# Kernel optimization log

Measured on AMD Instinct MI355X. Metric: run time of the kernel, lower is better.

## Reference

```python
import jax, jax.numpy as jnp
import numpy as np
from jax import lax

LEVEL = 128  # level_num

def _bn(x, g, b, m, v):
    # inference-mode BatchNorm, channel axis = 1
    sh = (1, -1) + (1,) * (x.ndim - 2)
    return (x - m.reshape(sh)) * (g.reshape(sh) * lax.rsqrt(v.reshape(sh) + 1e-5)) + b.reshape(sh)

def _leaky(a):
    return jnp.where(a > 0, a, 0.01 * a)

def _l2n(a):
    return a / jnp.maximum(jnp.linalg.norm(a, axis=1, keepdims=True), 1e-12)

def _resize_bilinear_ac(x, oh, ow):
    # bilinear, align_corners=True, NCHW
    n, c, h, w = x.shape
    ys = jnp.linspace(0.0, h - 1.0, oh)
    xs = jnp.linspace(0.0, w - 1.0, ow)
    y0 = jnp.floor(ys).astype(jnp.int32)
    x0 = jnp.floor(xs).astype(jnp.int32)
    y1 = jnp.minimum(y0 + 1, h - 1)
    x1 = jnp.minimum(x0 + 1, w - 1)
    wy = (ys - y0)[:, None]
    wx = (xs - x0)[None, :]
    Y0, Y1, X0, X1 = y0[:, None], y1[:, None], x0[None, :], x1[None, :]
    return (x[:, :, Y0, X0] * (1 - wy) * (1 - wx) + x[:, :, Y0, X1] * (1 - wy) * wx
            + x[:, :, Y1, X0] * wy * (1 - wx) + x[:, :, Y1, X1] * wy * wx)

def _forward(x, conv1_w, bn1_g, bn1_b, bn1_m, bn1_v, conv2_w, f1_w, f2_w, f2_g, f2_b, f2_m, f2_v,
             out1_w, out1_g, out1_b, out1_m, out1_v, k_w, q_w, v_w, out_w, out_g, out_b, out_m, out_v):
    # conv1: 3x3 conv + BN + LeakyReLU
    y = lax.conv_general_dilated(x, conv1_w, (1, 1), 'SAME', dimension_numbers=('NCHW', 'OIHW', 'NCHW'))
    y = _leaky(_bn(y, bn1_g, bn1_b, bn1_m, bn1_v))
    # conv2: 1x1 conv, 256->128
    x2 = jnp.einsum('nchw,oc->nohw', y, conv2_w)
    N, C, H, W = x2.shape  # C = 128
    x_ave = x2.mean(axis=(2, 3), keepdims=True)  # [N,C,1,1]
    cos = (_l2n(x_ave) * _l2n(x2)).sum(1)        # [N,H,W]
    sh, sw = H // 3, W // 3
    L = sh * sw
    # H,W divisible by 3 -> adaptive_avg_pool2d is identity
    cs = cos.reshape(N, 3, sh, 3, sw).transpose(0, 1, 3, 2, 4).reshape(N, 9, L).transpose(0, 2, 1)  # [N,L,9]
    # LBP bit packing vs center (index 4); weight 0 at index 4 (strict > gives 0 there)
    bits = (cs > cs[:, :, 4:5]).astype(x.dtype)
    wts = jnp.array([1, 2, 4, 8, 0, 16, 32, 64, 128], dtype=x.dtype)
    code = (bits * wts).sum(-1)  # [N,L]
    mn = code.min(-1, keepdims=True)
    mx = code.max(-1, keepdims=True)
    code = (code - mn) / (mx - mn)
    cmin = code.min(-1, keepdims=True)
    cmax = code.max(-1, keepdims=True)
    qlv = (2 * jnp.arange(LEVEL, dtype=x.dtype) + 1) / (2 * LEVEL) * (cmax - cmin) + cmin  # [N,LEVEL]
    inter = (qlv[:, 1] - qlv[:, 0])[:, None, None]  # [N,1,1]
    quant = 1 - jnp.abs(qlv[:, None, :] - code[:, :, None])  # [N,L,LEVEL]
    quant = jnp.where(quant > 1 - inter, quant, 0.0)
    sta = quant.sum(1)                                       # [N,LEVEL]
    sta = sta / sta.sum(-1, keepdims=True)
    sta2 = jnp.stack([qlv, sta], axis=1)                     # [N,2,LEVEL]
    h1 = _leaky(jnp.einsum('ncl,oc->nol', sta2, f1_w))       # f1: 2->64
    h2 = jax.nn.relu(_bn(jnp.einsum('ncl,oc->nol', h1, f2_w), f2_g, f2_b, f2_m, f2_v))  # f2: 64->128
    xa = jnp.broadcast_to(x_ave[:, :, 0, 0][:, :, None], (N, C, LEVEL))
    s = jnp.concatenate([h2, xa], axis=1)                    # [N,256,LEVEL]
    s = jax.nn.relu(_bn(jnp.einsum('ncl,oc->nol', s, out1_w), out1_g, out1_b, out1_m, out1_v))
    k = jnp.einsum('ncl,oc->nol', s, k_w)
    q = jnp.einsum('ncl,oc->nol', s, q_w)
    v = jnp.einsum('ncl,oc->nol', s, v_w)
    w = jax.nn.softmax(jnp.einsum('ncl,ncm->nlm', k, q), axis=-1)  # bmm(k^T, q)
    f = jnp.einsum('nlm,ncm->ncl', w, v)                            # bmm(w, v^T) then transpose
    f = jax.nn.relu(_bn(jnp.einsum('ncl,oc->nol', f, out_w), out_g, out_b, out_m, out_v))
    out = jnp.einsum('ncl,npl->ncp', f, quant).reshape(N, 256, sh, sh)  # bmm(f, quant^T)
    return _resize_bilinear_ac(out, H, W)

def setup_inputs() -> dict:
    key = jax.random.key(0)
    ks = jax.random.split(key, 16)
    f32 = jnp.float32
    def nrm(k, shape, s=0.05):
        return s * jax.random.normal(k, shape, f32)
    def bnp(k, c):
        k1, k2, k3, k4 = jax.random.split(k, 4)
        return (1.0 + 0.1 * jax.random.normal(k1, (c,), f32),
                0.1 * jax.random.normal(k2, (c,), f32),
                0.1 * jax.random.normal(k3, (c,), f32),
                jax.random.uniform(k4, (c,), f32, 0.5, 1.5))
    d = {}
    d['x'] = jax.random.normal(ks[0], (32, 512, 48, 48), f32)
    d['conv1_w'] = nrm(ks[1], (256, 512, 3, 3))
    d['bn1_g'], d['bn1_b'], d['bn1_m'], d['bn1_v'] = bnp(ks[2], 256)
    d['conv2_w'] = nrm(ks[3], (128, 256))
    d['f1_w'] = nrm(ks[4], (64, 2), 0.3)
    d['f2_w'] = nrm(ks[5], (128, 64), 0.1)
    d['f2_g'], d['f2_b'], d['f2_m'], d['f2_v'] = bnp(ks[6], 128)
    d['out1_w'] = nrm(ks[7], (256, 256))
    d['out1_g'], d['out1_b'], d['out1_m'], d['out1_v'] = bnp(ks[8], 256)
    d['k_w'] = nrm(ks[9], (256, 256))
    d['q_w'] = nrm(ks[10], (256, 256))
    d['v_w'] = nrm(ks[11], (256, 256))
    d['out_w'] = nrm(ks[12], (256, 256))
    d['out_g'], d['out_b'], d['out_m'], d['out_v'] = bnp(ks[13], 256)
    return d

def reference(x, conv1_w, bn1_g, bn1_b, bn1_m, bn1_v, conv2_w, f1_w, f2_w, f2_g, f2_b, f2_m, f2_v,
              out1_w, out1_g, out1_b, out1_m, out1_v, k_w, q_w, v_w, out_w, out_g, out_b, out_m, out_v):
    return _forward(x, conv1_w, bn1_g, bn1_b, bn1_m, bn1_v, conv2_w, f1_w, f2_w, f2_g, f2_b, f2_m, f2_v,
                    out1_w, out1_g, out1_b, out1_m, out1_v, k_w, q_w, v_w, out_w, out_g, out_b, out_m, out_v)
```

## Files before the change

### kernel.cpp

```cpp
#include <hip/hip_runtime.h>
#include <math.h>

#define N_IMG 32
#define P2304 2304
#define CIN 512
#define CMID 256
#define C2 128
#define LEV 128

typedef _Float16 half8 __attribute__((ext_vector_type(8)));
typedef float f32x16 __attribute__((ext_vector_type(16)));
typedef unsigned short u16;
typedef unsigned int u32;

__device__ __forceinline__ float wredSum(float v){
#pragma unroll
  for (int o = 32; o > 0; o >>= 1) v += __shfl_down(v, o, 64);
  return v;
}
__device__ __forceinline__ float wredMax(float v){
#pragma unroll
  for (int o = 32; o > 0; o >>= 1) v = fmaxf(v, __shfl_down(v, o, 64));
  return v;
}
__device__ __forceinline__ float wredMin(float v){
#pragma unroll
  for (int o = 32; o > 0; o >>= 1) v = fminf(v, __shfl_down(v, o, 64));
  return v;
}

__device__ __forceinline__ void gll16(const void* g, void* l){
  __builtin_amdgcn_global_load_lds(
      (const __attribute__((address_space(1))) void*)g,
      (__attribute__((address_space(3))) void*)l, 16, 0, 0);
}

__global__ void prep_w1_kernel(const float* __restrict__ w1,
                               uint4* __restrict__ Wh, uint4* __restrict__ Wl){
  int fid = blockIdx.x * 256 + threadIdx.x;
  int lam = fid & 63;
  int c32 = (fid >> 6) & 3;
  int cot = (fid >> 8) & 1;
  int kt  = fid >> 9;
  int co = cot * 128 + c32 * 32 + (lam & 31);
  half8 vh, vl;
#pragma unroll
  for (int j = 0; j < 8; ++j){
    int k = kt * 16 + ((lam >> 5) << 3) + j;
    int r = k >> 9;
    int ci = k & 511;
    float v = w1[co * (CIN * 9) + ci * 9 + r];
    _Float16 h = (_Float16)v;
    vh[j] = h;
    vl[j] = (_Float16)((v - (float)h) * 2048.0f);
  }
  Wh[fid] = *(uint4*)&vh;
  Wl[fid] = *(uint4*)&vl;
}

__global__ void prep_w2_kernel(const float* __restrict__ w2,
                               uint4* __restrict__ Wh, uint4* __restrict__ Wl){
  int fid = blockIdx.x * 256 + threadIdx.x;
  int lam = fid & 63;
  int c32 = (fid >> 6) & 3;
  int kt  = fid >> 8;
  int co = c32 * 32 + (lam & 31);
  half8 vh, vl;
#pragma unroll
  for (int j = 0; j < 8; ++j){
    int k = kt * 16 + ((lam >> 5) << 3) + j;
    float v = w2[co * CMID + k];
    _Float16 h = (_Float16)v;
    vh[j] = h;
    vl[j] = (_Float16)((v - (float)h) * 2048.0f);
  }
  Wh[fid] = *(uint4*)&vh;
  Wl[fid] = *(uint4*)&vl;
}

__global__ void prep_bn_kernel(const float* __restrict__ g1, const float* __restrict__ b1,
                               const float* __restrict__ m1, const float* __restrict__ v1,
                               float* __restrict__ s1, float* __restrict__ t1){
  int c = threadIdx.x;
  float s = g1[c] * (1.0f / sqrtf(v1[c] + 1e-5f));
  s1[c] = s;
  t1[c] = b1[c] - m1[c] * s;
}

__global__ void prep_x_kernel(const float* __restrict__ x,
                              u16* __restrict__ xh, u16* __restrict__ xl,
                              int n0){
  __shared__ float tile[128 * 49];
  const int t = threadIdx.x;
  const int b = blockIdx.x;
  const int n_loc = b / 50;
  const int hp = b - n_loc * 50;
  const int n = n0 + n_loc;
  const int h = hp - 1;
  const bool vrow = (h >= 0) && (h < 48);
  const size_t orow = ((size_t)n_loc * 50 + hp) * 50 * 512;
  for (int cc = 0; cc < 4; ++cc){
    if (vrow){
      const float* src = x + (((size_t)n * 512 + cc * 128) * 48 + h) * 48;
#pragma unroll
      for (int i = 0; i < 24; ++i){
        int idx = t + 256 * i;
        int w = idx % 48;
        int c = idx / 48;
        tile[c * 49 + w] = src[(size_t)c * 2304 + w];
      }
    }
    __syncthreads();
    for (int i = 0; i < 13; ++i){
      int idx = t + 256 * i;
      if (idx < 3200){
        int cpair = idx & 63;
        int wp = idx >> 6;
        int w = wp - 1;
        float v0 = 0.f, v1 = 0.f;
        if (vrow && (unsigned)w < 48u){
          v0 = tile[(cpair * 2) * 49 + w];
          v1 = tile[(cpair * 2 + 1) * 49 + w];
        }
        _Float16 h0 = (_Float16)v0, h1 = (_Float16)v1;
        _Float16 l0 = (_Float16)((v0 - (float)h0) * 2048.0f);
        _Float16 l1 = (_Float16)((v1 - (float)h1) * 2048.0f);
        union { _Float16 hh[2]; u32 uu; } ph, pl;
        ph.hh[0] = h0; ph.hh[1] = h1;
        pl.hh[0] = l0; pl.hh[1] = l1;
        ((u32*)(xh + orow + (size_t)wp * 512 + cc * 128))[cpair] = ph.uu;
        ((u32*)(xl + orow + (size_t)wp * 512 + cc * 128))[cpair] = pl.uu;
      }
    }
    __syncthreads();
  }
}

template<int NC>
__global__ __launch_bounds__(256, 2) void conv1_lds_kernel(
    const u16* __restrict__ xh, const u16* __restrict__ xl,
    const uint4* __restrict__ Wh, const uint4* __restrict__ Wl,
    const float* __restrict__ s1, const float* __restrict__ t1,
    float* __restrict__ out, int n0)
{
  __shared__ _Float16 Abuf[2][2][2][2048];
  __shared__ _Float16 Bbuf[2][2][2][2048];
  const int t = threadIdx.x;
  const int lam = t & 63;
  const int g = t >> 6;

  const int xcd = blockIdx.x & 7;
  const int rest = blockIdx.x >> 3;
  const int NPX = NC / 8;
  const int n_loc = xcd * NPX + rest / 36;
  const int inner = rest % 36;
  const int pt_blk = inner % 18;
  const int cot = inner / 18;
  const int n = n0 + n_loc;

  const int pbase = pt_blk * 128;
  const int khi = lam >> 5;
  const int pp = (g << 5) + (lam & 31);
  const int p = pbase + pp;
  const int ph = p / 48, pw = p - ph * 48;
  const u16* xh_n = xh + (size_t)n_loc * 1280000;
  const u16* xl_n = xl + (size_t)n_loc * 1280000;

  const int S = 144;

  f32x16 acc_hh[2][2], acc_x[2][2];
#pragma unroll
  for (int a = 0; a < 2; ++a)
#pragma unroll
    for (int b = 0; b < 2; ++b){
#pragma unroll
      for (int e = 0; e < 16; ++e){ acc_hh[a][b][e] = 0.f; acc_x[a][b][e] = 0.f; }
    }

#define ISSUE_L(SV, BUF)                                                      \
  {                                                                           \
    int s_ = (SV);                                                            \
    int k0_ = 2 * s_;                                                         \
    _Pragma("unroll")                                                         \
    for (int kf = 0; kf < 2; ++kf){                                           \
      int fg_ = ((k0_ + kf) * 2 + cot) * 4 + g;                               \
      gll16(Wh + fg_ * 64 + lam, &Abuf[BUF][kf][0][t * 8]);                   \
      gll16(Wl + fg_ * 64 + lam, &Abuf[BUF][kf][1][t * 8]);                   \
    }                                                                         \
    int r_ = k0_ >> 5;                                          \
    int cb_ = (k0_ & 31) << 4;                       \
    int hh_ = ph + r_ / 3;                                    \
    int ww_ = pw + r_ % 3;                                    \
    const u16* sh_ = xh_n + ((hh_ * 50 + ww_) << 9) + cb_ + (khi << 3);       \
    const u16* sl_ = xl_n + ((hh_ * 50 + ww_) << 9) + cb_ + (khi << 3);       \
    _Pragma("unroll")                                                         \
    for (int kf = 0; kf < 2; ++kf){                                           \
      gll16(sh_ + kf * 16, &Bbuf[BUF][kf][0][t * 8]);                         \
      gll16(sl_ + kf * 16, &Bbuf[BUF][kf][1][t * 8]);                         \
    }                                                                         \
  }

#define COMPUTE_L(CUR, KF)                                                    \
  {                                                                           \
    const int ct0 = (g & 1) * 2, pt0 = (g >> 1) * 2;                          \
    half8 fAh[2], fAl[2], fBh[2], fBl[2];                                     \
    _Pragma("unroll")                                                         \
    for (int a = 0; a < 2; ++a){                                              \
      fAh[a] = *(half8*)&Abuf[CUR][KF][0][(ct0 + a) * 512 + lam * 8];         \
      fAl[a] = *(half8*)&Abuf[CUR][KF][1][(ct0 + a) * 512 + lam * 8];         \
      fBh[a] = *(half8*)&Bbuf[CUR][KF][0][(pt0 + a) * 512 + lam * 8];         \
      fBl[a] = *(half8*)&Bbuf[CUR][KF][1][(pt0 + a) * 512 + lam * 8];         \
    }                                                                         \
    _Pragma("unroll")                                                         \
    for (int a = 0; a < 2; ++a)                                               \
      _Pragma("unroll")                                                       \
      for (int b = 0; b < 2; ++b){                                            \
        acc_hh[a][b] = __builtin_amdgcn_mfma_f32_32x32x16_f16(                \
            fAh[a], fBh[b], acc_hh[a][b], 0, 0, 0);                           \
        acc_x[a][b] = __builtin_amdgcn_mfma_f32_32x32x16_f16(                 \
            fAh[a], fBl[b], acc_x[a][b], 0, 0, 0);                            \
        acc_x[a][b] = __builtin_amdgcn_mfma_f32_32x32x16_f16(                 \
            fAl[a], fBh[b], acc_x[a][b], 0, 0, 0);                            \
      }                                                                       \
  }

  ISSUE_L(0, 0);
  __syncthreads();

  for (int s = 0; s < S; ++s){
    const int cur = s & 1;
    if (s + 1 < S) ISSUE_L(s + 1, cur ^ 1);
    COMPUTE_L(cur, 0);
    COMPUTE_L(cur, 1);
    __syncthreads();
  }
#undef ISSUE_L
#undef COMPUTE_L

  const int cobase = cot * 128;
#pragma unroll
  for (int a = 0; a < 2; ++a){
    const int ctile = (g & 1) * 2 + a;
#pragma unroll
    for (int b = 0; b < 2; ++b){
      const int ptile = (g >> 1) * 2 + b;
      const int pg = pbase + ptile * 32 + (lam & 31);
#pragma unroll
      for (int rg = 0; rg < 16; ++rg){
        const int row = (rg & 3) + 8 * (rg >> 2) + 4 * (lam >> 5);
        const int co = cobase + ctile * 32 + row;
        float val = acc_hh[a][b][rg] + acc_x[a][b][rg] * (1.0f / 2048.0f);
        val = val * s1[co] + t1[co];
        val = val > 0.f ? val : 0.01f * val;
        out[((size_t)n * 256 + co) * P2304 + pg] = val;
      }
    }
  }
}

template<int R, int CPT, int COTN, bool BN>
__global__ __launch_bounds__(256, 2) void conv_mfma_kernel(
    const float* __restrict__ in, const uint4* __restrict__ Wh, const uint4* __restrict__ Wl,
    const float* __restrict__ s1, const float* __restrict__ t1, float* __restrict__ out)
{
  __shared__ _Float16 Abuf[2][2][2][2048];
  __shared__ _Float16 Bbuf[2][2][2][2048];
  const int t = threadIdx.x;
  const int lam = t & 63;
  const int g = t >> 6;

  int n, pt_blk, cot;
  if (COTN == 2){
    int xcd = blockIdx.x & 7;
    int rest = blockIdx.x >> 3;
    n = xcd * 4 + rest / 36;
    int inner = rest % 36;
    pt_blk = inner % 18;
    cot = inner / 18;
  } else {
    pt_blk = blockIdx.x % 18;
    cot = 0;
    n = blockIdx.x / 18;
  }
  const int pbase = pt_blk * 128;
  const int cobase = cot * 128;

  const int khi = lam >> 5;
  const int pp = (g << 5) + (lam & 31);
  const int p = pbase + pp;
  const int ph = p / 48, pw = p - ph * 48;
  const float* in_n = in + (size_t)n * CPT * P2304;

  const int S = (R * CPT) / 32;
  const int KTPT = CPT / 16;

  f32x16 acc_hh[2][2], acc_x[2][2];
#pragma unroll
  for (int a = 0; a < 2; ++a)
#pragma unroll
    for (int b = 0; b < 2; ++b){
#pragma unroll
      for (int e = 0; e < 16; ++e){ acc_hh[a][b][e] = 0.f; acc_x[a][b][e] = 0.f; }
    }

  uint4 rAh[2], rAl[2];
  float rB[16];
  bool vmask;

#define ISSUE(SV)                                                             \
  {                                                                           \
    int s_ = (SV);                                                            \
    _Pragma("unroll")                                                         \
    for (int kf = 0; kf < 2; ++kf){                                           \
      int fi = (((2 * s_ + kf) * COTN + cot) * 4 + g) * 64 + lam;             \
      rAh[kf] = Wh[fi];                                                       \
      rAl[kf] = Wl[fi];                                                       \
    }                                                                         \
    int r_ = (R == 1) ? 0 : ((2 * s_) / KTPT);                                \
    int cbase_ = ((2 * s_) % KTPT) * 16;                                      \
    int dh_ = (R == 1) ? 0 : (r_ / 3 - 1);                                    \
    int dw_ = (R == 1) ? 0 : (r_ - (r_ / 3) * 3 - 1);                         \
    int hh_ = ph + dh_, ww_ = pw + dw_;                                       \
    vmask = ((unsigned)hh_ < 48u) & ((unsigned)ww_ < 48u);                    \
    int hc_ = min(max(hh_, 0), 47), wc_ = min(max(ww_, 0), 47);               \
    const float* src_ = in_n + hc_ * 48 + wc_                                 \
                        + (size_t)(cbase_ + khi * 8) * P2304;                 \
    _Pragma("unroll")                                                         \
    for (int kf = 0; kf < 2; ++kf)                                            \
      _Pragma("unroll")                                                       \
      for (int j = 0; j < 8; ++j)                                             \
        rB[kf * 8 + j] = src_[(kf * 16 + j) * P2304];                         \
  }

#define STASH(NXT)                                                            \
  {                                                                           \
    _Pragma("unroll")                                                         \
    for (int kf = 0; kf < 2; ++kf){                                           \
      *(uint4*)&Abuf[NXT][kf][0][t * 8] = rAh[kf];                            \
      *(uint4*)&Abuf[NXT][kf][1][t * 8] = rAl[kf];                            \
      half8 vh, vl;                                                           \
      _Pragma("unroll")                                                       \
      for (int j = 0; j < 8; ++j){                                            \
        float v = vmask ? rB[kf * 8 + j] : 0.0f;                              \
        _Float16 h = (_Float16)v;                                             \
        vh[j] = h;                                                            \
        vl[j] = (_Float16)((v - (float)h) * 2048.0f);                         \
      }                                                                       \
      *(half8*)&Bbuf[NXT][kf][0][t * 8] = vh;                                 \
      *(half8*)&Bbuf[NXT][kf][1][t * 8] = vl;                                 \
    }                                                                         \
  }

#define COMPUTE(CUR, KF)                                                      \
  {                                                                           \
    const int ct0 = (g & 1) * 2, pt0 = (g >> 1) * 2;                          \
    half8 fAh[2], fAl[2], fBh[2], fBl[2];                                     \
    _Pragma("unroll")                                                         \
    for (int a = 0; a < 2; ++a){                                              \
      fAh[a] = *(half8*)&Abuf[CUR][KF][0][(ct0 + a) * 512 + lam * 8];         \
      fAl[a] = *(half8*)&Abuf[CUR][KF][1][(ct0 + a) * 512 + lam * 8];         \
      fBh[a] = *(half8*)&Bbuf[CUR][KF][0][(pt0 + a) * 512 + lam * 8];         \
      fBl[a] = *(half8*)&Bbuf[CUR][KF][1][(pt0 + a) * 512 + lam * 8];         \
    }                                                                         \
    _Pragma("unroll")                                                         \
    for (int a = 0; a < 2; ++a)                                               \
      _Pragma("unroll")                                                       \
      for (int b = 0; b < 2; ++b){                                            \
        acc_hh[a][b] = __builtin_amdgcn_mfma_f32_32x32x16_f16(                \
            fAh[a], fBh[b], acc_hh[a][b], 0, 0, 0);                           \
        acc_x[a][b] = __builtin_amdgcn_mfma_f32_32x32x16_f16(                 \
            fAh[a], fBl[b], acc_x[a][b], 0, 0, 0);                            \
        acc_x[a][b] = __builtin_amdgcn_mfma_f32_32x32x16_f16(                 \
            fAl[a], fBh[b], acc_x[a][b], 0, 0, 0);                            \
      }                                                                       \
  }

  ISSUE(0);
  STASH(0);
  __syncthreads();

  for (int s = 0; s < S; ++s){
    const int cur = s & 1, nxt = cur ^ 1;
    const bool more = (s + 1 < S);
    if (more) ISSUE(s + 1);
    COMPUTE(cur, 0);
    if (more) STASH(nxt);
    COMPUTE(cur, 1);
    __syncthreads();
  }
#undef ISSUE
#undef STASH
#undef COMPUTE

  const int M = COTN * 128;
#pragma unroll
  for (int a = 0; a < 2; ++a){
    const int ctile = (g & 1) * 2 + a;
#pragma unroll
    for (int b = 0; b < 2; ++b){
      const int ptile = (g >> 1) * 2 + b;
      const int pg = pbase + ptile * 32 + (lam & 31);
#pragma unroll
      for (int rg = 0; rg < 16; ++rg){
        const int row = (rg & 3) + 8 * (rg >> 2) + 4 * (lam >> 5);
        const int co = cobase + ctile * 32 + row;
        float val = acc_hh[a][b][rg] + acc_x[a][b][rg] * (1.0f / 2048.0f);
        if (BN){
          val = val * s1[co] + t1[co];
          val = val > 0.f ? val : 0.01f * val;
        }
        out[((size_t)n * M + co) * P2304 + pg] = val;
      }
    }
  }
}

__global__ void xave_kernel(const float* __restrict__ x2, float* __restrict__ xave){
  __shared__ float red[4];
  int nc = blockIdx.x, t = threadIdx.x;
  const float* row = x2 + nc * P2304;
  float s = 0.f;
#pragma unroll
  for (int i = 0; i < 9; i++) s += row[t + 256 * i];
  float w = wredSum(s);
  if ((t & 63) == 0) red[t >> 6] = w;
  __syncthreads();
  if (t == 0) xave[nc] = (red[0] + red[1] + red[2] + red[3]) * (1.0f / 2304.0f);
}

__global__ void xan_kernel(const float* __restrict__ xave, float* __restrict__ xan){
  __shared__ float red[2];
  int n = blockIdx.x, t = threadIdx.x;
  float v = xave[n * 128 + t];
  float w = wredSum(v * v);
  if ((t & 63) == 0) red[t >> 6] = w;
  __syncthreads();
  float norm = fmaxf(sqrtf(red[0] + red[1]), 1e-12f);
  xan[n * 128 + t] = v / norm;
}

__global__ void cos_kernel(const float* __restrict__ x2, const float* __restrict__ xan,
                           float* __restrict__ cosb){
  int idx = blockIdx.x * 256 + threadIdx.x;
  if (idx >= N_IMG * P2304) return;
  int n = idx / P2304;
  int p = idx - n * P2304;
  const float* xp = x2 + n * C2 * P2304 + p;
  const float* an = xan + n * 128;
  float dot = 0.f, ss = 0.f;
  for (int c = 0; c < 128; c++){
    float v = xp[c * P2304];
    dot += an[c] * v;
    ss  += v * v;
  }
  cosb[idx] = dot / fmaxf(sqrtf(ss), 1e-12f);
}

__global__ void lbp_kernel(const float* __restrict__ cosb, float* __restrict__ code,
                           float* __restrict__ qlv){
  __shared__ float red[4];
  int n = blockIdx.x;
  int l = threadIdx.x;
  int ir = l >> 4, ic = l & 15;
  const float* cn = cosb + n * P2304;
  float cs4 = cn[(16 + ir) * 48 + (16 + ic)];
  const float wts[9] = {1.f, 2.f, 4.f, 8.f, 0.f, 16.f, 32.f, 64.f, 128.f};
  float codev = 0.f;
#pragma unroll
  for (int j = 0; j < 9; j++){
    int jr = j / 3, jc = j - 3 * (j / 3);
    float vv = cn[(jr * 16 + ir) * 48 + (jc * 16 + ic)];
    if (vv > cs4) codev += wts[j];
  }
  float w;
  w = wredMin(codev);
  if ((l & 63) == 0) red[l >> 6] = w;
  __syncthreads();
  float mn = fminf(fminf(red[0], red[1]), fminf(red[2], red[3]));
  __syncthreads();
  w = wredMax(codev);
  if ((l & 63) == 0) red[l >> 6] = w;
  __syncthreads();
  float mx = fmaxf(fmaxf(red[0], red[1]), fmaxf(red[2], red[3]));
  __syncthreads();
  float cd = (codev - mn) / (mx - mn);
  w = wredMin(cd);
  if ((l & 63) == 0) red[l >> 6] = w;
  __syncthreads();
  float cmin = fminf(fminf(red[0], red[1]), fminf(red[2], red[3]));
  __syncthreads();
  w = wredMax(cd);
  if ((l & 63) == 0) red[l >> 6] = w;
  __syncthreads();
  float cmax = fmaxf(fmaxf(red[0], red[1]), fmaxf(red[2], red[3]));
  code[n * 256 + l] = cd;
  if (l < 128){
    float tmp = (float)(2 * l + 1) * (1.0f / 256.0f);
    qlv[n * 128 + l] = tmp * (cmax - cmin) + cmin;
  }
}

__global__ void quant_kernel(const float* __restrict__ code, const float* __restrict__ qlv,
                             float* __restrict__ quantT){
  __shared__ float cs[256];
  __shared__ float qs[128];
  int n = blockIdx.x, t = threadIdx.x;
  cs[t] = code[n * 256 + t];
  if (t < 128) qs[t] = qlv[n * 128 + t];
  __syncthreads();
  float thr = 1.0f - (qs[1] - qs[0]);
  float* dst = quantT + n * LEV * 256;
#pragma unroll 4
  for (int i = 0; i < 128; i++){
    int v = t + 256 * i;
    int lv = v >> 8;
    int p = v & 255;
    float qq = 1.0f - fabsf(qs[lv] - cs[p]);
    dst[v] = (qq > thr) ? qq : 0.f;
  }
}

__global__ void sta_kernel(const float* __restrict__ quantT, float* __restrict__ sta){
  __shared__ float red[2];
  int n = blockIdx.x, i = threadIdx.x;
  const float* qr = quantT + (n * LEV + i) * 256;
  float s = 0.f;
  for (int p = 0; p < 256; p++) s += qr[p];
  float w = wredSum(s);
  if ((i & 63) == 0) red[i >> 6] = w;
  __syncthreads();
  float tot = red[0] + red[1];
  sta[n * 128 + i] = s / tot;
}

__global__ void h1_kernel(const float* __restrict__ f1w, const float* __restrict__ qlv,
                          const float* __restrict__ sta, float* __restrict__ h1){
  int idx = blockIdx.x * 256 + threadIdx.x;
  if (idx >= N_IMG * 64 * 128) return;
  int l = idx & 127;
  int n = idx >> 13;
  int o = (idx >> 7) & 63;
  float a = f1w[o * 2] * qlv[n * 128 + l] + f1w[o * 2 + 1] * sta[n * 128 + l];
  h1[idx] = a > 0.f ? a : 0.01f * a;
}

__global__ void gemm_w_kernel(const float* __restrict__ Wm, const float* __restrict__ B,
                              float* __restrict__ Cout, int Cdim, int O, int total, int mode,
                              const float* __restrict__ g, const float* __restrict__ bb,
                              const float* __restrict__ mm, const float* __restrict__ vv){
  int idx = blockIdx.x * 256 + threadIdx.x;
  if (idx >= total) return;
  int per_n = (O >> 2) << 7;
  int n = idx / per_n;
  int rem = idx - n * per_n;
  int o0 = (rem >> 7) << 2;
  int l = rem & 127;
  const float* Bn = B + (n * Cdim) * 128 + l;
  const float* w0 = Wm + (o0 + 0) * Cdim;
  const float* w1 = Wm + (o0 + 1) * Cdim;
  const float* w2 = Wm + (o0 + 2) * Cdim;
  const float* w3 = Wm + (o0 + 3) * Cdim;
  float a0 = 0, a1 = 0, a2 = 0, a3 = 0;
  for (int c = 0; c < Cdim; c++){
    float bv = Bn[c * 128];
    a0 += w0[c] * bv; a1 += w1[c] * bv; a2 += w2[c] * bv; a3 += w3[c] * bv;
  }
  float av[4] = {a0, a1, a2, a3};
#pragma unroll
  for (int j = 0; j < 4; j++){
    int o = o0 + j;
    float val = av[j];
    if (mode == 1){
      float s = g[o] * (1.0f / sqrtf(vv[o] + 1e-5f));
      val = (val - mm[o]) * s + bb[o];
      val = fmaxf(val, 0.f);
    }
    Cout[(n * O + o) * 128 + l] = val;
  }
}

__global__ void concat_kernel(const float* __restrict__ h2, const float* __restrict__ xave,
                              float* __restrict__ s){
  int idx = blockIdx.x * 256 + threadIdx.x;
  if (idx >= N_IMG * 256 * 128) return;
  int l = idx & 127;
  int c = (idx >> 7) & 255;
  int n = idx >> 15;
  s[idx] = (c < 128) ? h2[(n * 128 + c) * 128 + l] : xave[n * 128 + (c - 128)];
}

__global__ void attn_sc_kernel(const float* __restrict__ k, const float* __restrict__ q,
                               float* __restrict__ sc){
  int idx = blockIdx.x * 256 + threadIdx.x;
  if (idx >= N_IMG * 32 * 128) return;
  int m = idx & 127;
  int l0 = ((idx >> 7) & 31) << 2;
  int n = idx >> 12;
  const float* kn = k + n * 256 * 128;
  const float* qn = q + n * 256 * 128 + m;
  float a0 = 0, a1 = 0, a2 = 0, a3 = 0;
  for (int c = 0; c < 256; c++){
    float qv = qn[c * 128];
    const float* kr = kn + c * 128 + l0;
    a0 += kr[0] * qv; a1 += kr[1] * qv; a2 += kr[2] * qv; a3 += kr[3] * qv;
  }
  float* dst = sc + (n * 128 + l0) * 128 + m;
  dst[0] = a0; dst[128] = a1; dst[256] = a2; dst[384] = a3;
}

__global__ void softmax_kernel(float* __restrict__ sc){
  __shared__ float red[2];
  int row = blockIdx.x;
  int t = threadIdx.x;
  float v = sc[row * 128 + t];
  float w = wredMax(v);
  if ((t & 63) == 0) red[t >> 6] = w;
  __syncthreads();
  float mx = fmaxf(red[0], red[1]);
  float e = expf(v - mx);
  float s = wredSum(e);
  __syncthreads();
  if ((t & 63) == 0) red[t >> 6] = s;
  __syncthreads();
  sc[row * 128 + t] = e / (red[0] + red[1]);
}

__global__ void transpose_sc_kernel(const float* __restrict__ sc, float* __restrict__ scT){
  int idx = blockIdx.x * 256 + threadIdx.x;
  if (idx >= N_IMG * 128 * 128) return;
  int l = idx & 127;
  int m = (idx >> 7) & 127;
  int n = idx >> 14;
  scT[idx] = sc[(n * 128 + l) * 128 + m];
}

__global__ void attn_f_kernel(const float* __restrict__ vb, const float* __restrict__ scT,
                              float* __restrict__ f){
  int idx = blockIdx.x * 256 + threadIdx.x;
  if (idx >= N_IMG * 64 * 128) return;
  int l = idx & 127;
  int c0 = ((idx >> 7) & 63) << 2;
  int n = idx >> 13;
  const float* vn = vb + (n * 256 + c0) * 128;
  const float* sn = scT + n * 128 * 128 + l;
  float a0 = 0, a1 = 0, a2 = 0, a3 = 0;
  for (int m = 0; m < 128; m++){
    float sv = sn[m * 128];
    a0 += vn[m] * sv; a1 += vn[128 + m] * sv; a2 += vn[256 + m] * sv; a3 += vn[384 + m] * sv;
  }
  float* dst = f + (n * 256 + c0) * 128 + l;
  dst[0] = a0; dst[128] = a1; dst[256] = a2; dst[384] = a3;
}

__global__ void final_kernel(const float* __restrict__ g, const float* __restrict__ quantT,
                             float* __restrict__ outs){
  int idx = blockIdx.x * 256 + threadIdx.x;
  if (idx >= N_IMG * 64 * 256) return;
  int p = idx & 255;
  int c0 = ((idx >> 8) & 63) << 2;
  int n = idx >> 14;
  const float* gn = g + (n * 256 + c0) * 128;
  const float* qn = quantT + (n * LEV) * 256 + p;
  float a0 = 0, a1 = 0, a2 = 0, a3 = 0;
  for (int lv = 0; lv < 128; lv++){
    float qv = qn[lv * 256];
    a0 += gn[lv] * qv; a1 += gn[128 + lv] * qv; a2 += gn[256 + lv] * qv; a3 += gn[384 + lv] * qv;
  }
  float* dst = outs + (n * 256 + c0) * 256 + p;
  dst[0] = a0; dst[256] = a1; dst[512] = a2; dst[768] = a3;
}

__global__ void resize_kernel(const float* __restrict__ outs, float* __restrict__ dout){
  int idx = blockIdx.x * 256 + threadIdx.x;
  if (idx >= N_IMG * 256 * P2304) return;
  int ow = idx % 48;
  int tmp = idx / 48;
  int oh = tmp % 48;
  int nc = tmp / 48;
  const float* src = outs + nc * 256;
  float fy = oh * (15.0f / 47.0f);
  float fx = ow * (15.0f / 47.0f);
  int y0 = (int)fy;
  int x0 = (int)fx;
  int y1 = min(y0 + 1, 15);
  int x1 = min(x0 + 1, 15);
  float wy = fy - (float)y0;
  float wx = fx - (float)x0;
  float v00 = src[y0 * 16 + x0], v01 = src[y0 * 16 + x1];
  float v10 = src[y1 * 16 + x0], v11 = src[y1 * 16 + x1];
  dout[idx] = v00 * (1.f - wy) * (1.f - wx) + v01 * (1.f - wy) * wx
            + v10 * wy * (1.f - wx) + v11 * wy * wx;
}

extern "C" void kernel_launch(void* const* d_in, const int* in_sizes, int n_in,
                              void* d_out, int out_size, void* d_ws, size_t ws_size,
                              hipStream_t stream)
{
  const float* x       = (const float*)d_in[0];
  const float* conv1_w = (const float*)d_in[1];
  const float* bn1_g   = (const float*)d_in[2];
  const float* bn1_b   = (const float*)d_in[3];
  const float* bn1_m   = (const float*)d_in[4];
  const float* bn1_v   = (const float*)d_in[5];
  const float* conv2_w = (const float*)d_in[6];
  const float* f1_w    = (const float*)d_in[7];
  const float* f2_w    = (const float*)d_in[8];
  const float* f2_g    = (const float*)d_in[9];
  const float* f2_b    = (const float*)d_in[10];
  const float* f2_m    = (const float*)d_in[11];
  const float* f2_v    = (const float*)d_in[12];
  const float* out1_w  = (const float*)d_in[13];
  const float* out1_g  = (const float*)d_in[14];
  const float* out1_b  = (const float*)d_in[15];
  const float* out1_m  = (const float*)d_in[16];
  const float* out1_v  = (const float*)d_in[17];
  const float* k_w     = (const float*)d_in[18];
  const float* q_w     = (const float*)d_in[19];
  const float* v_w     = (const float*)d_in[20];
  const float* out_w   = (const float*)d_in[21];
  const float* out_g   = (const float*)d_in[22];
  const float* out_b   = (const float*)d_in[23];
  const float* out_m   = (const float*)d_in[24];
  const float* out_v   = (const float*)d_in[25];

  float* ws = (float*)d_ws;
  float* dout = (float*)d_out;

  float* w_y   = ws;
  float* w_x2  = ws + 18874368;
  float* w_W1h = ws + 28311552;
  float* w_W1l = ws + 28901376;
  float* w_W2h = ws + 29491200;
  float* w_W2l = ws + 29507584;
  float* w_s1  = ws + 29523968;
  float* w_t1  = ws + 29524224;
  float* w_xave = w_y + 0;
  float* w_xan  = w_y + 4096;
  float* w_cos  = w_y + 8192;
  float* w_code = w_y + 81920;
  float* w_qlv  = w_y + 90112;
  float* w_sta  = w_y + 94208;
  float* w_quant= w_y + 98304;
  float* w_h1   = w_y + 1146880;
  float* w_h2   = w_y + 1409024;
  float* w_s    = w_y + 1933312;
  float* w_k    = w_y + 2981888;
  float* w_q    = w_y + 4030464;
  float* w_v    = w_y + 5079040;
  float* w_sc   = w_y + 6127616;
  float* w_scT  = w_y + 6651904;
  float* w_f    = w_y + 7176192;
  float* w_g    = w_y + 8224768;
  float* w_outs = w_y + 9273344;
  float* w_s2   = w_y + 11370496;

  prep_w1_kernel<<<576, 256, 0, stream>>>(conv1_w, (uint4*)w_W1h, (uint4*)w_W1l);
  prep_w2_kernel<<<16, 256, 0, stream>>>(conv2_w, (uint4*)w_W2h, (uint4*)w_W2l);
  prep_bn_kernel<<<1, 256, 0, stream>>>(bn1_g, bn1_b, bn1_m, bn1_v, w_s1, w_t1);

  const size_t BASE_F = 29524480;
  const size_t XPI_F  = 640000;
  const size_t ws_f = ws_size / 4;
  int NCc = 0;
  if (ws_f >= BASE_F + 2 * 32 * XPI_F)      NCc = 32;
  else if (ws_f >= BASE_F + 2 * 16 * XPI_F) NCc = 16;

  if (NCc > 0){
    u16* w_xh = (u16*)(ws + BASE_F);
    u16* w_xl = w_xh + (size_t)NCc * 1280000;
    const int nchunk = N_IMG / NCc;
    for (int c = 0; c < nchunk; ++c){
      int n0 = c * NCc;
      prep_x_kernel<<<NCc * 50, 256, 0, stream>>>(x, w_xh, w_xl, n0);
      if (NCc == 32)
        conv1_lds_kernel<32><<<1152, 256, 0, stream>>>(
            w_xh, w_xl, (const uint4*)w_W1h, (const uint4*)w_W1l, w_s1, w_t1, w_y, n0);
      else
        conv1_lds_kernel<16><<<576, 256, 0, stream>>>(
            w_xh, w_xl, (const uint4*)w_W1h, (const uint4*)w_W1l, w_s1, w_t1, w_y, n0);
    }
  } else {
    conv_mfma_kernel<9, 512, 2, true><<<1152, 256, 0, stream>>>(
        x, (const uint4*)w_W1h, (const uint4*)w_W1l, w_s1, w_t1, w_y);
  }

  conv_mfma_kernel<1, 256, 1, false><<<576, 256, 0, stream>>>(
      w_y, (const uint4*)w_W2h, (const uint4*)w_W2l, w_s1, w_t1, w_x2);

  xave_kernel<<<4096, 256, 0, stream>>>(w_x2, w_xave);
  xan_kernel<<<32, 128, 0, stream>>>(w_xave, w_xan);
  cos_kernel<<<288, 256, 0, stream>>>(w_x2, w_xan, w_cos);
  lbp_kernel<<<32, 256, 0, stream>>>(w_cos, w_code, w_qlv);
  quant_kernel<<<32, 256, 0, stream>>>(w_code, w_qlv, w_quant);
  sta_kernel<<<32, 128, 0, stream>>>(w_quant, w_sta);
  h1_kernel<<<1024, 256, 0, stream>>>(f1_w, w_qlv, w_sta, w_h1);
  gemm_w_kernel<<<512, 256, 0, stream>>>(f2_w, w_h1, w_h2, 64, 128, N_IMG * 32 * 128, 1,
                                         f2_g, f2_b, f2_m, f2_v);
  concat_kernel<<<4096, 256, 0, stream>>>(w_h2, w_xave, w_s);
  gemm_w_kernel<<<1024, 256, 0, stream>>>(out1_w, w_s, w_s2, 256, 256, N_IMG * 64 * 128, 1,
                                          out1_g, out1_b, out1_m, out1_v);
  gemm_w_kernel<<<1024, 256, 0, stream>>>(k_w, w_s2, w_k, 256, 256, N_IMG * 64 * 128, 0,
                                          nullptr, nullptr, nullptr, nullptr);
  gemm_w_kernel<<<1024, 256, 0, stream>>>(q_w, w_s2, w_q, 256, 256, N_IMG * 64 * 128, 0,
                                          nullptr, nullptr, nullptr, nullptr);
  gemm_w_kernel<<<1024, 256, 0, stream>>>(v_w, w_s2, w_v, 256, 256, N_IMG * 64 * 128, 0,
                                          nullptr, nullptr, nullptr, nullptr);
  attn_sc_kernel<<<512, 256, 0, stream>>>(w_k, w_q, w_sc);
  softmax_kernel<<<4096, 128, 0, stream>>>(w_sc);
  transpose_sc_kernel<<<2048, 256, 0, stream>>>(w_sc, w_scT);
  attn_f_kernel<<<1024, 256, 0, stream>>>(w_v, w_scT, w_f);
  gemm_w_kernel<<<1024, 256, 0, stream>>>(out_w, w_f, w_g, 256, 256, N_IMG * 64 * 128, 1,
                                          out_g, out_b, out_m, out_v);
  final_kernel<<<2048, 256, 0, stream>>>(w_g, w_quant, w_outs);
  resize_kernel<<<73728, 256, 0, stream>>>(w_outs, dout);
}
```

Before: 1.736 ms.

## Deepen conv1 pipeline to 4 stages and emit split-fp16 NHWC for new conv2 kernel

The conv1 LDS kernel moves from a double-buffered loop with full __syncthreads to a four-slot ring. It prefetches two steps ahead, waits on explicit vmcnt counters with raw barriers, and raises wave priority around the MFMA block. The conv1 epilogue now writes its output as hi/lo fp16 pairs in pixel-major layout instead of fp32 NCHW. A new conv2 kernel then streams those pairs straight into LDS with direct global-to-LDS loads, removing the per-element fp32-to-fp16 split and staging conversion. This trades more LDS per block and hand-tuned wait counts, which are fragile, for better latency hiding and less conversion work between the two convolutions.

```diff
diff --git a/kernel.cpp b/kernel.cpp
--- a/kernel.cpp
+++ b/kernel.cpp
@@ -136,71 +136,7 @@
   }
 }
 
-template<int NC>
-__global__ __launch_bounds__(256, 2) void conv1_lds_kernel(
-    const u16* __restrict__ xh, const u16* __restrict__ xl,
-    const uint4* __restrict__ Wh, const uint4* __restrict__ Wl,
-    const float* __restrict__ s1, const float* __restrict__ t1,
-    float* __restrict__ out, int n0)
-{
-  __shared__ _Float16 Abuf[2][2][2][2048];
-  __shared__ _Float16 Bbuf[2][2][2][2048];
-  const int t = threadIdx.x;
-  const int lam = t & 63;
-  const int g = t >> 6;
-
-  const int xcd = blockIdx.x & 7;
-  const int rest = blockIdx.x >> 3;
-  const int NPX = NC / 8;
-  const int n_loc = xcd * NPX + rest / 36;
-  const int inner = rest % 36;
-  const int pt_blk = inner % 18;
-  const int cot = inner / 18;
-  const int n = n0 + n_loc;
-
-  const int pbase = pt_blk * 128;
-  const int khi = lam >> 5;
-  const int pp = (g << 5) + (lam & 31);
-  const int p = pbase + pp;
-  const int ph = p / 48, pw = p - ph * 48;
-  const u16* xh_n = xh + (size_t)n_loc * 1280000;
-  const u16* xl_n = xl + (size_t)n_loc * 1280000;
-
-  const int S = 144;
-
-  f32x16 acc_hh[2][2], acc_x[2][2];
-#pragma unroll
-  for (int a = 0; a < 2; ++a)
-#pragma unroll
-    for (int b = 0; b < 2; ++b){
-#pragma unroll
-      for (int e = 0; e < 16; ++e){ acc_hh[a][b][e] = 0.f; acc_x[a][b][e] = 0.f; }
-    }
-
-#define ISSUE_L(SV, BUF)                                                      \
-  {                                                                           \
-    int s_ = (SV);                                                            \
-    int k0_ = 2 * s_;                                                         \
-    _Pragma("unroll")                                                         \
-    for (int kf = 0; kf < 2; ++kf){                                           \
-      int fg_ = ((k0_ + kf) * 2 + cot) * 4 + g;                               \
-      gll16(Wh + fg_ * 64 + lam, &Abuf[BUF][kf][0][t * 8]);                   \
-      gll16(Wl + fg_ * 64 + lam, &Abuf[BUF][kf][1][t * 8]);                   \
-    }                                                                         \
-    int r_ = k0_ >> 5;                                          \
-    int cb_ = (k0_ & 31) << 4;                       \
-    int hh_ = ph + r_ / 3;                                    \
-    int ww_ = pw + r_ % 3;                                    \
-    const u16* sh_ = xh_n + ((hh_ * 50 + ww_) << 9) + cb_ + (khi << 3);       \
-    const u16* sl_ = xl_n + ((hh_ * 50 + ww_) << 9) + cb_ + (khi << 3);       \
-    _Pragma("unroll")                                                         \
-    for (int kf = 0; kf < 2; ++kf){                                           \
-      gll16(sh_ + kf * 16, &Bbuf[BUF][kf][0][t * 8]);                         \
-      gll16(sl_ + kf * 16, &Bbuf[BUF][kf][1][t * 8]);                         \
-    }                                                                         \
-  }
-
-#define COMPUTE_L(CUR, KF)                                                    \
+#define COMPUTE_M(CUR, KF)                                                    \
   {                                                                           \
     const int ct0 = (g & 1) * 2, pt0 = (g >> 1) * 2;                          \
     half8 fAh[2], fAl[2], fBh[2], fBl[2];                                     \
@@ -224,18 +160,100 @@
       }                                                                       \
   }
 
-  ISSUE_L(0, 0);
-  __syncthreads();
-
-  for (int s = 0; s < S; ++s){
-    const int cur = s & 1;
-    if (s + 1 < S) ISSUE_L(s + 1, cur ^ 1);
-    COMPUTE_L(cur, 0);
-    COMPUTE_L(cur, 1);
-    __syncthreads();
-  }
-#undef ISSUE_L
-#undef COMPUTE_L
+#define WAITV16 asm volatile("s_waitcnt vmcnt(16)" ::: "memory")
+#define WAITV8  asm volatile("s_waitcnt vmcnt(8)"  ::: "memory")
+#define WAITV0  asm volatile("s_waitcnt vmcnt(0)"  ::: "memory")
+#define BARSB { __builtin_amdgcn_s_barrier(); __builtin_amdgcn_sched_barrier(0); }
+
+template<int NC>
+__global__ __launch_bounds__(256, 2) void conv1_lds_kernel(
+    const u16* __restrict__ xh, const u16* __restrict__ xl,
+    const uint4* __restrict__ Wh, const uint4* __restrict__ Wl,
+    const float* __restrict__ s1, const float* __restrict__ t1,
+    u16* __restrict__ yh, u16* __restrict__ yl, int n0)
+{
+  __shared__ _Float16 Abuf[4][2][2][2048];
+  __shared__ _Float16 Bbuf[4][2][2][2048];
+  const int t = threadIdx.x;
+  const int lam = t & 63;
+  const int g = t >> 6;
+
+  const int xcd = blockIdx.x & 7;
+  const int rest = blockIdx.x >> 3;
+  const int NPX = NC / 8;
+  const int n_loc = xcd * NPX + rest / 36;
+  const int inner = rest % 36;
+  const int pt_blk = inner % 18;
+  const int cot = inner / 18;
+  const int n = n0 + n_loc;
+
+  const int pbase = pt_blk * 128;
+  const int khi = lam >> 5;
+  const int pp = (g << 5) + (lam & 31);
+  const int p = pbase + pp;
+  const int ph = p / 48, pw = p - ph * 48;
+  const u16* xh_n = xh + (size_t)n_loc * 1280000;
+  const u16* xl_n = xl + (size_t)n_loc * 1280000;
+
+  const int S = 144;
+
+  f32x16 acc_hh[2][2], acc_x[2][2];
+#pragma unroll
+  for (int a = 0; a < 2; ++a)
+#pragma unroll
+    for (int b = 0; b < 2; ++b){
+#pragma unroll
+      for (int e = 0; e < 16; ++e){ acc_hh[a][b][e] = 0.f; acc_x[a][b][e] = 0.f; }
+    }
+
+#define ISSUE1(SV, BUF)                                                       \
+  {                                                                           \
+    int s_ = (SV);                                                            \
+    int k0_ = 2 * s_;                                                         \
+    _Pragma("unroll")                                                         \
+    for (int kf = 0; kf < 2; ++kf){                                           \
+      int fg_ = ((k0_ + kf) * 2 + cot) * 4 + g;                               \
+      gll16(Wh + fg_ * 64 + lam, &Abuf[BUF][kf][0][t * 8]);                   \
+      gll16(Wl + fg_ * 64 + lam, &Abuf[BUF][kf][1][t * 8]);                   \
+    }                                                                         \
+    int r_ = k0_ >> 5;                                          \
+    int cb_ = (k0_ & 31) << 4;                       \
+    int hh_ = ph + r_ / 3;                                    \
+    int ww_ = pw + r_ % 3;                                    \
+    const u16* sh_ = xh_n + ((hh_ * 50 + ww_) << 9) + cb_ + (khi << 3);       \
+    const u16* sl_ = xl_n + ((hh_ * 50 + ww_) << 9) + cb_ + (khi << 3);       \
+    _Pragma("unroll")                                                         \
+    for (int kf = 0; kf < 2; ++kf){                                           \
+      gll16(sh_ + kf * 16, &Bbuf[BUF][kf][0][t * 8]);                         \
+      gll16(sl_ + kf * 16, &Bbuf[BUF][kf][1][t * 8]);                         \
+    }                                                                         \
+  }
+
+  ISSUE1(0, 0);
+  ISSUE1(1, 1);
+
+  for (int s = 0; s < S - 2; ++s){
+    ISSUE1(s + 2, (s + 2) & 3);
+    WAITV16;
+    BARSB;
+    __builtin_amdgcn_s_setprio(1);
+    COMPUTE_M(s & 3, 0);
+    COMPUTE_M(s & 3, 1);
+    __builtin_amdgcn_s_setprio(0);
+  }
+  WAITV8;
+  BARSB;
+  __builtin_amdgcn_s_setprio(1);
+  COMPUTE_M((S - 2) & 3, 0);
+  COMPUTE_M((S - 2) & 3, 1);
+  __builtin_amdgcn_s_setprio(0);
+  WAITV0;
+  BARSB;
+  __builtin_amdgcn_s_setprio(1);
+  COMPUTE_M((S - 1) & 3, 0);
+  COMPUTE_M((S - 1) & 3, 1);
+  __builtin_amdgcn_s_setprio(0);
+#undef ISSUE1
 
   const int cobase = cot * 128;
 #pragma unroll
@@ -245,14 +263,117 @@
     for (int b = 0; b < 2; ++b){
       const int ptile = (g >> 1) * 2 + b;
       const int pg = pbase + ptile * 32 + (lam & 31);
+      u16* dh = yh + (((size_t)n * P2304 + pg) << 8);
+      u16* dl = yl + (((size_t)n * P2304 + pg) << 8);
+#pragma unroll
+      for (int q = 0; q < 4; ++q){
+        const int co0 = cobase + ctile * 32 + 8 * q + 4 * khi;
+        union { _Float16 h[4]; uint2 u; } Uh, Ul;
+#pragma unroll
+        for (int i = 0; i < 4; ++i){
+          const int rg = 4 * q + i;
+          const int co = co0 + i;
+          float val = acc_hh[a][b][rg] + acc_x[a][b][rg] * (1.0f / 2048.0f);
+          val = val * s1[co] + t1[co];
+          val = val > 0.f ? val : 0.01f * val;
+          _Float16 h = (_Float16)val;
+          Uh.h[i] = h;
+          Ul.h[i] = (_Float16)((val - (float)h) * 2048.0f);
+        }
+        *(uint2*)(dh + co0) = Uh.u;
+        *(uint2*)(dl + co0) = Ul.u;
+      }
+    }
+  }
+}
+
+__global__ __launch_bounds__(256, 2) void conv2_lds_kernel(
+    const u16* __restrict__ yh, const u16* __restrict__ yl,
+    const uint4* __restrict__ Wh, const uint4* __restrict__ Wl,
+    float* __restrict__ out)
+{
+  __shared__ _Float16 Abuf[4][2][2][2048];
+  __shared__ _Float16 Bbuf[4][2][2][2048];
+  const int t = threadIdx.x;
+  const int lam = t & 63;
+  const int g = t >> 6;
+
+  const int pt_blk = blockIdx.x % 18;
+  const int n = blockIdx.x / 18;
+  const int pbase = pt_blk * 128;
+  const int khi = lam >> 5;
+  const int p = pbase + (g << 5) + (lam & 31);
+  const u16* yh_n = yh + (size_t)n * P2304 * 256;
+  const u16* yl_n = yl + (size_t)n * P2304 * 256;
+
+  const int S = 8;
+
+  f32x16 acc_hh[2][2], acc_x[2][2];
+#pragma unroll
+  for (int a = 0; a < 2; ++a)
+#pragma unroll
+    for (int b = 0; b < 2; ++b){
+#pragma unroll
+      for (int e = 0; e < 16; ++e){ acc_hh[a][b][e] = 0.f; acc_x[a][b][e] = 0.f; }
+    }
+
+#define ISSUE2(SV, BUF)                                                       \
+  {                                                                           \
+    int s_ = (SV);                                                            \
+    _Pragma("unroll")                                                         \
+    for (int kf = 0; kf < 2; ++kf){                                           \
+      int fg_ = (2 * s_ + kf) * 4 + g;                                        \
+      gll16(Wh + fg_ * 64 + lam, &Abuf[BUF][kf][0][t * 8]);                   \
+      gll16(Wl + fg_ * 64 + lam, &Abuf[BUF][kf][1][t * 8]);                   \
+    }                                                                         \
+    const u16* sh_ = yh_n + ((size_t)p << 8) + (s_ << 5) + (khi << 3);        \
+    const u16* sl_ = yl_n + ((size_t)p << 8) + (s_ << 5) + (khi << 3);        \
+    _Pragma("unroll")                                                         \
+    for (int kf = 0; kf < 2; ++kf){                                           \
+      gll16(sh_ + kf * 16, &Bbuf[BUF][kf][0][t * 8]);                         \
+      gll16(sl_ + kf * 16, &Bbuf[BUF][kf][1][t * 8]);                         \
+    }                                                                         \
+  }
+
+  ISSUE2(0, 0);
+  ISSUE2(1, 1);
+
+  for (int s = 0; s < S - 2; ++s){
+    ISSUE2(s + 2, (s + 2) & 3);
+    WAITV16;
+    BARSB;
+    __builtin_amdgcn_s_setprio(1);
+    COMPUTE_M(s & 3, 0);
+    COMPUTE_M(s & 3, 1);
+    __builtin_amdgcn_s_setprio(0);
+  }
+  WAITV8;
+  BARSB;
+  __builtin_amdgcn_s_setprio(1);
+  COMPUTE_M((S - 2) & 3, 0);
+  COMPUTE_M((S - 2) & 3, 1);
+  __builtin_amdgcn_s_setprio(0);
+  WAITV0;
+  BARSB;
+  __builtin_amdgcn_s_setprio(1);
+  COMPUTE_M((S - 1) & 3, 0);
+  COMPUTE_M((S - 1) & 3, 1);
+  __builtin_amdgcn_s_setprio(0);
+#undef ISSUE2
+
+#pragma unroll
+  for (int a = 0; a < 2; ++a){
+    const int ctile = (g & 1) * 2 + a;
+#pragma unroll
+    for (int b = 0; b < 2; ++b){
+      const int ptile = (g >> 1) * 2 + b;
+      const int pg = pbase + ptile * 32 + (lam & 31);
 #pragma unroll
       for (int rg = 0; rg < 16; ++rg){
-        const int row = (rg & 3) + 8 * (rg >> 2) + 4 * (lam >> 5);
-        const int co = cobase + ctile * 32 + row;
+        const int row = (rg & 3) + 8 * (rg >> 2) + 4 * khi;
+        const int co = ctile * 32 + row;
         float val = acc_hh[a][b][rg] + acc_x[a][b][rg] * (1.0f / 2048.0f);
-        val = val * s1[co] + t1[co];
-        val = val > 0.f ? val : 0.01f * val;
-        out[((size_t)n * 256 + co) * P2304 + pg] = val;
+        out[((size_t)n * C2 + co) * P2304 + pg] = val;
       }
     }
   }
@@ -344,37 +465,13 @@
         float v = vmask ? rB[kf * 8 + j] : 0.0f;                              \
         _Float16 h = (_Float16)v;                                             \
         vh[j] = h;                                                            \
-        vl[j] = (_Float16)((v - (float)h) * 2048.0f);                         \
+        vl[j] = (_Float16)((v - (float)h) * 2048.0f);                        \
       }                                                                       \
       *(half8*)&Bbuf[NXT][kf][0][t * 8] = vh;                                 \
       *(half8*)&Bbuf[NXT][kf][1][t * 8] = vl;                                 \
     }                                                                         \
   }
 
-#define COMPUTE(CUR, KF)                                                      \
-  {                                                                           \
-    const int ct0 = (g & 1) * 2, pt0 = (g >> 1) * 2;                          \
-    half8 fAh[2], fAl[2], fBh[2], fBl[2];                                     \
-    _Pragma("unroll")                                                         \
-    for (int a = 0; a < 2; ++a){                                              \
-      fAh[a] = *(half8*)&Abuf[CUR][KF][0][(ct0 + a) * 512 + lam * 8];         \
-      fAl[a] = *(half8*)&Abuf[CUR][KF][1][(ct0 + a) * 512 + lam * 8];         \
-      fBh[a] = *(half8*)&Bbuf[CUR][KF][0][(pt0 + a) * 512 + lam * 8];         \
-      fBl[a] = *(half8*)&Bbuf[CUR][KF][1][(pt0 + a) * 512 + lam * 8];         \
-    }                                                                         \
-    _Pragma("unroll")                                                         \
-    for (int a = 0; a < 2; ++a)                                               \
-      _Pragma("unroll")                                                       \
-      for (int b = 0; b < 2; ++b){                                            \
-        acc_hh[a][b] = __builtin_amdgcn_mfma_f32_32x32x16_f16(                \
-            fAh[a], fBh[b], acc_hh[a][b], 0, 0, 0);                           \
-        acc_x[a][b] = __builtin_amdgcn_mfma_f32_32x32x16_f16(                 \
-            fAh[a], fBl[b], acc_x[a][b], 0, 0, 0);                            \
-        acc_x[a][b] = __builtin_amdgcn_mfma_f32_32x32x16_f16(                 \
-            fAl[a], fBh[b], acc_x[a][b], 0, 0, 0);                            \
-      }                                                                       \
-  }
-
   ISSUE(0);
   STASH(0);
   __syncthreads();
@@ -383,14 +480,13 @@
     const int cur = s & 1, nxt = cur ^ 1;
     const bool more = (s + 1 < S);
     if (more) ISSUE(s + 1);
-    COMPUTE(cur, 0);
+    COMPUTE_M(cur, 0);
     if (more) STASH(nxt);
-    COMPUTE(cur, 1);
+    COMPUTE_M(cur, 1);
     __syncthreads();
   }
 #undef ISSUE
 #undef STASH
-#undef COMPUTE
 
   const int M = COTN * 128;
 #pragma unroll
@@ -768,24 +864,29 @@
   if (NCc > 0){
     u16* w_xh = (u16*)(ws + BASE_F);
     u16* w_xl = w_xh + (size_t)NCc * 1280000;
+    u16* w_yh = (u16*)w_y;
+    u16* w_yl = (u16*)(w_y + 9437184);
     const int nchunk = N_IMG / NCc;
     for (int c = 0; c < nchunk; ++c){
       int n0 = c * NCc;
       prep_x_kernel<<<NCc * 50, 256, 0, stream>>>(x, w_xh, w_xl, n0);
       if (NCc == 32)
         conv1_lds_kernel<32><<<1152, 256, 0, stream>>>(
-            w_xh, w_xl, (const uint4*)w_W1h, (const uint4*)w_W1l, w_s1, w_t1, w_y, n0);
+            w_xh, w_xl, (const uint4*)w_W1h, (const uint4*)w_W1l, w_s1, w_t1,
+            w_yh, w_yl, n0);
       else
         conv1_lds_kernel<16><<<576, 256, 0, stream>>>(
-            w_xh, w_xl, (const uint4*)w_W1h, (const uint4*)w_W1l, w_s1, w_t1, w_y, n0);
+            w_xh, w_xl, (const uint4*)w_W1h, (const uint4*)w_W1l, w_s1, w_t1,
+            w_yh, w_yl, n0);
     }
+    conv2_lds_kernel<<<576, 256, 0, stream>>>(
+        w_yh, w_yl, (const uint4*)w_W2h, (const uint4*)w_W2l, w_x2);
   } else {
     conv_mfma_kernel<9, 512, 2, true><<<1152, 256, 0, stream>>>(
         x, (const uint4*)w_W1h, (const uint4*)w_W1l, w_s1, w_t1, w_y);
-  }
-
-  conv_mfma_kernel<1, 256, 1, false><<<576, 256, 0, stream>>>(
-      w_y, (const uint4*)w_W2h, (const uint4*)w_W2l, w_s1, w_t1, w_x2);
+    conv_mfma_kernel<1, 256, 1, false><<<576, 256, 0, stream>>>(
+        w_y, (const uint4*)w_W2h, (const uint4*)w_W2l, w_s1, w_t1, w_x2);
+  }
 
   xave_kernel<<<4096, 256, 0, stream>>>(w_x2, w_xave);
   xan_kernel<<<32, 128, 0, stream>>>(w_xave, w_xan);
```

Result: slower. 1.774 ms (+2.1%).
